# Performance work log

Hardware: AMD Instinct MI355X
Metric: run time of the kernel (lower is better)

Reference implementation:

```python
import jax, jax.numpy as jnp
import numpy as np

ACT_BITS = 8
W_BITS = 8
BN_EPS = 1e-5


def _round_ste(x):
    # straight-through round (HAWQ-style ste_round)
    return x + jax.lax.stop_gradient(jnp.round(x) - x)


def _quant_sym(x, bits):
    # symmetric per-tensor fake quantization; scale treated as constant (EMA min/max in original)
    n = float(2 ** (bits - 1) - 1)
    s = jax.lax.stop_gradient(jnp.maximum(jnp.max(jnp.abs(x)) / n, 1e-8))
    xq = jnp.clip(_round_ste(x / s), -n - 1.0, n) * s
    return xq, s


def _conv(x, w, stride, pad):
    return jax.lax.conv_general_dilated(
        x, w, (stride, stride), [(pad, pad), (pad, pad)],
        dimension_numbers=("NCHW", "OIHW", "NCHW"))


def _quant_bn(x, gamma, beta, mean, var):
    # fold BN into a per-channel scale+bias; quantize the folded scale like a weight
    ws = gamma * jax.lax.rsqrt(var + BN_EPS)          # [C]
    wq, ws_scale = _quant_sym(ws, W_BITS)
    b = beta - mean * wq                               # [C]
    return x * wq[None, :, None, None] + b[None, :, None, None], ws_scale


def setup_inputs() -> dict:
    key = jax.random.key(0)
    ks = jax.random.split(key, 16)
    d = {}
    d["x"] = jax.random.normal(ks[0], (32, 128, 56, 56), jnp.float32)
    d["w1"] = jax.random.normal(ks[1], (256, 128, 3, 3), jnp.float32) * 0.05
    d["w2"] = jax.random.normal(ks[2], (256, 256, 3, 3), jnp.float32) * 0.05
    d["w_id"] = jax.random.normal(ks[3], (256, 128, 1, 1), jnp.float32) * 0.05
    for i, pfx in enumerate(["bn1", "bn2", "id"]):
        k4 = jax.random.split(ks[4 + i], 4)
        d[pfx + "_gamma"] = jax.random.uniform(k4[0], (256,), jnp.float32) + 0.5
        d[pfx + "_beta"] = jax.random.normal(k4[1], (256,), jnp.float32) * 0.1
        d[pfx + "_mean"] = jax.random.normal(k4[2], (256,), jnp.float32) * 0.1
        d[pfx + "_var"] = jax.random.uniform(k4[3], (256,), jnp.float32) + 0.5
    return d


def reference(x, w1, w2, w_id,
              bn1_gamma, bn1_beta, bn1_mean, bn1_var,
              bn2_gamma, bn2_beta, bn2_mean, bn2_var,
              id_gamma, id_beta, id_mean, id_var):
    # quant_act on block input
    xq, act_s = _quant_sym(x, ACT_BITS)

    # identity branch: 1x1 stride-2 quantized conv -> quant_act -> folded quant bn
    w_id_q, _ = _quant_sym(w_id, W_BITS)
    identity = _conv(xq, w_id_q, 2, 0)
    identity, _ = _quant_sym(identity, ACT_BITS)
    identity, _ = _quant_bn(identity, id_gamma, id_beta, id_mean, id_var)

    # main branch conv1 (3x3 stride 2) -> act quant -> bn -> relu -> act quant
    w1_q, _ = _quant_sym(w1, W_BITS)
    h = _conv(xq, w1_q, 2, 1)
    h, _ = _quant_sym(h, ACT_BITS)
    h, _ = _quant_bn(h, bn1_gamma, bn1_beta, bn1_mean, bn1_var)
    h = jax.nn.relu(h)
    h, _ = _quant_sym(h, ACT_BITS)

    # conv2 (3x3 stride 1) -> act quant -> bn
    w2_q, _ = _quant_sym(w2, W_BITS)
    h = _conv(h, w2_q, 1, 1)
    h, _ = _quant_sym(h, ACT_BITS)
    h, _ = _quant_bn(h, bn2_gamma, bn2_beta, bn2_mean, bn2_var)

    # residual add -> int32 requant -> relu
    h = h + identity
    h, out_s = _quant_sym(h, ACT_BITS)
    h = jax.nn.relu(h)
    return h, out_s
```

## Files before the change

### kernel.cpp

```cpp
#include <hip/hip_runtime.h>
#include <limits.h>

#define THREADS 256

typedef int vi4 __attribute__((ext_vector_type(4)));

__device__ __forceinline__ float clamp8f(float q) { return fminf(fmaxf(q, -128.0f), 127.0f); }
__device__ __forceinline__ float sc_from_bits(unsigned b) {
  return fmaxf(__uint_as_float(b) / 127.0f, 1e-8f);
}
__device__ __forceinline__ signed char q8(float v, float s) {
  return (signed char)(int)clamp8f(rintf(v / s));
}


__device__ __forceinline__ void amax_body(const float4* __restrict__ p, int n4, int bid,
                                          int nblocks, unsigned* __restrict__ slot) {
  const int tid = threadIdx.x;
  const int stride = nblocks * THREADS;
  float m = 0.0f;
  int i = bid * THREADS + tid;
  for (; i + 3 * stride < n4; i += 4 * stride) {
    float4 v0 = p[i];
    float4 v1 = p[i + stride];
    float4 v2 = p[i + 2 * stride];
    float4 v3 = p[i + 3 * stride];
    float m0 = fmaxf(fmaxf(fabsf(v0.x), fabsf(v0.y)), fmaxf(fabsf(v0.z), fabsf(v0.w)));
    float m1 = fmaxf(fmaxf(fabsf(v1.x), fabsf(v1.y)), fmaxf(fabsf(v1.z), fabsf(v1.w)));
    float m2 = fmaxf(fmaxf(fabsf(v2.x), fabsf(v2.y)), fmaxf(fabsf(v2.z), fabsf(v2.w)));
    float m3 = fmaxf(fmaxf(fabsf(v3.x), fabsf(v3.y)), fmaxf(fabsf(v3.z), fabsf(v3.w)));
    m = fmaxf(m, fmaxf(fmaxf(m0, m1), fmaxf(m2, m3)));
  }
  for (; i < n4; i += stride) {
    float4 v = p[i];
    m = fmaxf(m, fmaxf(fmaxf(fabsf(v.x), fabsf(v.y)), fmaxf(fabsf(v.z), fabsf(v.w))));
  }
#pragma unroll
  for (int k = 32; k >= 1; k >>= 1) m = fmaxf(m, __shfl_xor(m, k));
  __shared__ float wred[4];
  if ((tid & 63) == 0) wred[tid >> 6] = m;
  __syncthreads();
  if (tid == 0) {
    m = fmaxf(fmaxf(wred[0], wred[1]), fmaxf(wred[2], wred[3]));
    atomicMax(slot, __float_as_uint(m));
  }
}

__global__ __launch_bounds__(THREADS) void k_pre(
    int* IS, const float* g1, const float* be1, const float* m1, const float* v1, float* wq1,
    float* b1, const float* g2, const float* be2, const float* m2, const float* v2, float* wq2,
    float* b2, const float* gi, const float* bei, const float* mi, const float* vvi, float* wqi,
    float* bi, const float4* w1, const float4* w2, const float4* wid, const float4* x) {
  unsigned* ISu = (unsigned*)IS;
  int b = blockIdx.x;
  int c = threadIdx.x;
  if (b < 3) {
    const float *gamma, *beta, *mean, *var;
    float *wq, *bb;
    if (b == 0) { gamma = g1; beta = be1; mean = m1; var = v1; wq = wq1; bb = b1; }
    else if (b == 1) { gamma = g2; beta = be2; mean = m2; var = v2; wq = wq2; bb = b2; }
    else { gamma = gi; beta = bei; mean = mi; var = vvi; wq = wqi; bb = bi; }
    __shared__ float red[THREADS];
    float ws = gamma[c] * (1.0f / sqrtf(var[c] + 1e-5f));
    red[c] = fabsf(ws);
    __syncthreads();
    for (int s = THREADS / 2; s > 0; s >>= 1) {
      if (c < s) red[c] = fmaxf(red[c], red[c + s]);
      __syncthreads();
    }
    float sws = fmaxf(red[0] / 127.0f, 1e-8f);
    float q = clamp8f(rintf(ws / sws)) * sws;
    wq[c] = q;
    bb[c] = beta[c] - mean[c] * q;
    return;
  }
  b -= 3;
  if (b < 64) { amax_body(w1, 73728, b, 64, ISu + 1); return; }
  b -= 64;
  if (b < 128) { amax_body(w2, 147456, b, 128, ISu + 2); return; }
  b -= 128;
  if (b < 16) { amax_body(wid, 8192, b, 16, ISu + 3); return; }
  b -= 16;
  amax_body(x, 3211264, b, 512, ISu + 0);
}

__global__ __launch_bounds__(THREADS) void k_quant(const float* __restrict__ x,
                                                   int* __restrict__ X8,
                                                   const float* __restrict__ w1f,
                                                   vi4* __restrict__ W1m,
                                                   const float* __restrict__ w2f,
                                                   vi4* __restrict__ W2m,
                                                   const float* __restrict__ widf,
                                                   vi4* __restrict__ Widm,
                                                   const unsigned* __restrict__ ISu) {
  __shared__ signed char tile[56 * 132];
  int b = blockIdx.x;
  int t = threadIdx.x;
  if (b < 1792) {
    float s = sc_from_bits(ISu[0]);
    int h = b % 56, n = b / 56;
    const float* xp = x + ((n * 128) * 56 + h) * 56;
#pragma unroll
    for (int k = 0; k < 28; ++k) {
      int i = t + k * 256;
      int w = i % 56, c = i / 56;
      tile[w * 132 + c] = q8(xp[c * 3136 + w], s);
    }
    __syncthreads();
    int* op = X8 + (n * 56 + h) * 56 * 32;
#pragma unroll
    for (int k = 0; k < 7; ++k) {
      int i = t + k * 256;
      int w = i >> 5, c4 = (i & 31) * 4;
      const signed char* tp = tile + w * 132 + c4;
      op[i] = (int)(unsigned char)tp[0] | ((int)(unsigned char)tp[1] << 8) |
              ((int)(unsigned char)tp[2] << 16) | ((int)(unsigned char)tp[3] << 24);
    }
    return;
  }
  if (b < 1864) {
    int tt = (b - 1792) * THREADS + t;
    float s = sc_from_bits(ISu[1]);
    int lane = tt & 63;
    int cotile = (tt >> 6) & 15;
    int ks = tt >> 10;
    int tap = ks >> 1, kc = ks & 1;
    int kh = tap / 3, kw = tap % 3;
    int co = cotile * 16 + (lane & 15);
    int ci0 = kc * 64 + (lane >> 4) * 16;
    const float* src = w1f + (co * 128 + ci0) * 9 + kh * 3 + kw;
    int r[4];
#pragma unroll
    for (int q = 0; q < 4; ++q) {
      unsigned b0 = (unsigned char)q8(src[(q * 4 + 0) * 9], s);
      unsigned b1 = (unsigned char)q8(src[(q * 4 + 1) * 9], s);
      unsigned b2 = (unsigned char)q8(src[(q * 4 + 2) * 9], s);
      unsigned b3 = (unsigned char)q8(src[(q * 4 + 3) * 9], s);
      r[q] = (int)(b0 | (b1 << 8) | (b2 << 16) | (b3 << 24));
    }
    vi4 v = {r[0], r[1], r[2], r[3]};
    W1m[tt] = v;
    return;
  }
  if (b < 2008) {
    int tt = (b - 1864) * THREADS + t;
    float s = sc_from_bits(ISu[2]);
    int lane = tt & 63;
    int cotile = (tt >> 6) & 15;
    int ks = tt >> 10;
    int tap = ks >> 2, kc = ks & 3;
    int kh = tap / 3, kw = tap % 3;
    int co = cotile * 16 + (lane & 15);
    int ci0 = kc * 64 + (lane >> 4) * 16;
    const float* src = w2f + (co * 256 + ci0) * 9 + kh * 3 + kw;
    int r[4];
#pragma unroll
    for (int q = 0; q < 4; ++q) {
      unsigned b0 = (unsigned char)q8(src[(q * 4 + 0) * 9], s);
      unsigned b1 = (unsigned char)q8(src[(q * 4 + 1) * 9], s);
      unsigned b2 = (unsigned char)q8(src[(q * 4 + 2) * 9], s);
      unsigned b3 = (unsigned char)q8(src[(q * 4 + 3) * 9], s);
      r[q] = (int)(b0 | (b1 << 8) | (b2 << 16) | (b3 << 24));
    }
    vi4 v = {r[0], r[1], r[2], r[3]};
    W2m[tt] = v;
    return;
  }
  {
    int tt = (b - 2008) * THREADS + t;
    float s = sc_from_bits(ISu[3]);
    int lane = tt & 63;
    int cotile = (tt >> 6) & 15;
    int ks = tt >> 10;
    int co = cotile * 16 + (lane & 15);
    int ci0 = ks * 64 + (lane >> 4) * 16;
    const float* src = widf + co * 128 + ci0;
    int r[4];
#pragma unroll
    for (int q = 0; q < 4; ++q) {
      unsigned b0 = (unsigned char)q8(src[q * 4 + 0], s);
      unsigned b1 = (unsigned char)q8(src[q * 4 + 1], s);
      unsigned b2 = (unsigned char)q8(src[q * 4 + 2], s);
      unsigned b3 = (unsigned char)q8(src[q * 4 + 3], s);
      r[q] = (int)(b0 | (b1 << 8) | (b2 << 16) | (b3 << 24));
    }
    vi4 v = {r[0], r[1], r[2], r[3]};
    Widm[tt] = v;
  }
}

#define MFMA_I8(a, b, c) __builtin_amdgcn_mfma_i32_16x16x64_i8(a, b, c, 0, 0, 0)

__global__ __launch_bounds__(THREADS, 2) void k_conv1(const int* __restrict__ X8,
                                                      const vi4* __restrict__ W1m,
                                                      const vi4* __restrict__ Widm,
                                                      int* __restrict__ H1, int* __restrict__ IDI,
                                                      int* __restrict__ maxS,
                                                      int* __restrict__ minS,
                                                      int* __restrict__ maxabs_id) {
  __shared__ __align__(16) int lds[5 * 58 * 36];
  __shared__ int sMax[2][128], sMin[2][128], redA[4];
  const int tid = threadIdx.x;
  const int bx = blockIdx.x;
  const int n = bx / 28, rr = bx % 28;
  const int hp = rr >> 1, nh = rr & 1;
  const int ho0 = hp * 2;
  vi4 zero = {0, 0, 0, 0};

  for (int r = 0; r < 5; ++r) {
    int h = 2 * ho0 - 1 + r;
    int* dst = lds + r * 58 * 36;
    if (h >= 0 && h < 56) {
      const vi4* src = (const vi4*)(X8 + (n * 56 + h) * 56 * 32);
      for (int i4 = tid; i4 < 448; i4 += THREADS) {
        int col = i4 >> 3, c = (i4 & 7) * 4;
        *(vi4*)(dst + (col + 1) * 36 + c) = src[i4];
      }
      if (tid < 32) dst[tid] = 0;
      else if (tid >= 128 && tid < 160) dst[57 * 36 + (tid - 128)] = 0;
    } else {
      for (int i4 = tid; i4 < 522; i4 += THREADS) ((vi4*)dst)[i4] = zero;
    }
  }
  __syncthreads();

  const int lane = tid & 63, wv = tid >> 6;
  const int mw = wv & 1, nw = wv >> 1;
  const int lm = lane & 15, quad = lane >> 4;
  const int woc0 = lm, woc1 = (16 + lm) > 27 ? 27 : (16 + lm);
  const int choff = quad * 4;
  const int ho = ho0 + mw;
  const int obase = ((n * 28 + ho) * 28) * 256;
  const int ctbase = nh * 8 + nw * 4;

  vi4 acc[2][4];
  vi4 bcur[4], bnext[4];
  vi4 a0c, a1c, a0n, a1n;

#pragma unroll
  for (int mt = 0; mt < 2; ++mt)
#pragma unroll
    for (int ct = 0; ct < 4; ++ct) acc[mt][ct] = zero;
  const vi4* wibase = Widm + ctbase * 64 + lane;
  {
    const int ro = (2 * mw + 1) * 58;
#pragma unroll
    for (int kc = 0; kc < 2; ++kc) {
      vi4 a0 = *(const vi4*)(lds + (ro + 2 * woc0 + 1) * 36 + kc * 16 + choff);
      vi4 a1 = *(const vi4*)(lds + (ro + 2 * woc1 + 1) * 36 + kc * 16 + choff);
#pragma unroll
      for (int ct = 0; ct < 4; ++ct) {
        vi4 b = wibase[kc * 1024 + ct * 64];
        acc[0][ct] = MFMA_I8(a0, b, acc[0][ct]);
        acc[1][ct] = MFMA_I8(a1, b, acc[1][ct]);
      }
    }
  }
  int am = 0;
#pragma unroll
  for (int ct = 0; ct < 4; ++ct) {
    const int co = (ctbase + ct) * 16 + lm;
#pragma unroll
    for (int mt = 0; mt < 2; ++mt)
#pragma unroll
      for (int r = 0; r < 4; ++r) {
        int wo = mt * 16 + quad * 4 + r;
        if (wo < 28) {
          int v = acc[mt][ct][r];
          IDI[obase + wo * 256 + co] = v;
          am = max(am, v < 0 ? -v : v);
        }
      }
  }
#pragma unroll
  for (int k = 32; k >= 1; k >>= 1) am = max(am, __shfl_xor(am, k));
  if (lane == 0) redA[wv] = am;

#pragma unroll
  for (int mt = 0; mt < 2; ++mt)
#pragma unroll
    for (int ct = 0; ct < 4; ++ct) acc[mt][ct] = zero;
  const vi4* wbase = W1m + ctbase * 64 + lane;
#pragma unroll
  for (int ct = 0; ct < 4; ++ct) bcur[ct] = wbase[ct * 64];
  {
    const int ro = (2 * mw) * 58;
    a0c = *(const vi4*)(lds + (ro + 2 * woc0) * 36 + choff);
    a1c = *(const vi4*)(lds + (ro + 2 * woc1) * 36 + choff);
  }
#pragma unroll 1
  for (int ks = 0; ks < 18; ++ks) {
    int ksn = ks + 1;
    if (ksn < 18) {
      int khn = (ksn >= 6) + (ksn >= 12);
      int t2 = ksn - khn * 6;
      int kwn = t2 >> 1, kcn = t2 & 1;
#pragma unroll
      for (int ct = 0; ct < 4; ++ct) bnext[ct] = wbase[ksn * 1024 + ct * 64];
      int ro = (2 * mw + khn) * 58;
      a0n = *(const vi4*)(lds + (ro + 2 * woc0 + kwn) * 36 + kcn * 16 + choff);
      a1n = *(const vi4*)(lds + (ro + 2 * woc1 + kwn) * 36 + kcn * 16 + choff);
    }
#pragma unroll
    for (int ct = 0; ct < 4; ++ct) {
      acc[0][ct] = MFMA_I8(a0c, bcur[ct], acc[0][ct]);
      acc[1][ct] = MFMA_I8(a1c, bcur[ct], acc[1][ct]);
    }
    a0c = a0n;
    a1c = a1n;
#pragma unroll
    for (int ct = 0; ct < 4; ++ct) bcur[ct] = bnext[ct];
  }

#pragma unroll
  for (int ct = 0; ct < 4; ++ct) {
    const int co = (ctbase + ct) * 16 + lm;
    int vmax = INT_MIN, vmin = INT_MAX;
#pragma unroll
    for (int mt = 0; mt < 2; ++mt)
#pragma unroll
      for (int r = 0; r < 4; ++r) {
        int wo = mt * 16 + quad * 4 + r;
        if (wo < 28) {
          int v = acc[mt][ct][r];
          H1[obase + wo * 256 + co] = v;
          vmax = max(vmax, v);
          vmin = min(vmin, v);
        }
      }
    vmax = max(vmax, __shfl_xor(vmax, 16));
    vmax = max(vmax, __shfl_xor(vmax, 32));
    vmin = min(vmin, __shfl_xor(vmin, 16));
    vmin = min(vmin, __shfl_xor(vmin, 32));
    if (lane < 16) {
      sMax[mw][nw * 64 + ct * 16 + lane] = vmax;
      sMin[mw][nw * 64 + ct * 16 + lane] = vmin;
    }
  }
  __syncthreads();
  if (tid < 128) {
    int row = n * 14 + hp;
    maxS[row * 256 + nh * 128 + tid] = max(sMax[0][tid], sMax[1][tid]);
    minS[row * 256 + nh * 128 + tid] = min(sMin[0][tid], sMin[1][tid]);
  }
  if (tid == 0) {
    int a = max(max(redA[0], redA[1]), max(redA[2], redA[3]));
    atomicMax(maxabs_id, a);
  }
}

__global__ __launch_bounds__(THREADS) void k_rs1(int* __restrict__ IS, float* __restrict__ SC,
                                                 const int* __restrict__ maxS,
                                                 const int* __restrict__ minS,
                                                 const float* __restrict__ wq1,
                                                 const float* __restrict__ b1) {
  __shared__ int ri[THREADS];
  __shared__ float rf[THREADS];
  int c = threadIdx.x;
  int vmax = INT_MIN, vmin = INT_MAX;
#pragma unroll 4
  for (int r = 0; r < 448; ++r) {
    vmax = max(vmax, maxS[r * 256 + c]);
    vmin = min(vmin, minS[r * 256 + c]);
  }
  int a1 = vmax < 0 ? -vmax : vmax;
  int a0 = vmin < 0 ? -vmin : vmin;
  ri[c] = max(a1, a0);
  __syncthreads();
  for (int s = THREADS / 2; s > 0; s >>= 1) {
    if (c < s) ri[c] = max(ri[c], ri[c + s]);
    __syncthreads();
  }
  int mh1 = ri[0];
  const unsigned* ISu = (const unsigned*)IS;
  float sx = sc_from_bits(ISu[0]);
  float sw1 = sc_from_bits(ISu[1]);
  float sxw = sx * sw1;
  float s_h1 = fmaxf(sxw * (float)mh1 / 127.0f, 1e-8f);
  float wq = wq1[c], bbc = b1[c];
  float q1 = clamp8f(rintf((float)vmax * sxw / s_h1));
  float q0 = clamp8f(rintf((float)vmin * sxw / s_h1));
  float hv1 = q1 * s_h1, hv0 = q0 * s_h1;
  float y1 = fmaxf(hv1 * wq + bbc, 0.0f);
  float y0 = fmaxf(hv0 * wq + bbc, 0.0f);
  rf[c] = fmaxf(y1, y0);
  __syncthreads();
  for (int s = THREADS / 2; s > 0; s >>= 1) {
    if (c < s) rf[c] = fmaxf(rf[c], rf[c + s]);
    __syncthreads();
  }
  if (c == 0) {
    IS[4] = mh1;
    SC[7] = rf[0];
    SC[8] = s_h1;
    SC[9] = fmaxf(rf[0] / 127.0f, 1e-8f);
    float swid = sc_from_bits(ISu[3]);
    SC[10] = fmaxf(sx * swid * (float)IS[5] / 127.0f, 1e-8f);
  }
}

__device__ __forceinline__ signed char qact(int v, float sxw, float s_h1, float s_y2, float wq,
                                            float bb) {
  float hf = (float)v * sxw;
  float q = clamp8f(rintf(hf / s_h1));
  float hv = q * s_h1;
  float y = fmaxf(hv * wq + bb, 0.0f);
  float a = fminf(fmaxf(rintf(y / s_y2), -128.0f), 127.0f);
  return (signed char)(int)a;
}

__global__ __launch_bounds__(THREADS) void k_qh1(const int4* __restrict__ H1,
                                                 char4* __restrict__ A2,
                                                 const float* __restrict__ SC,
                                                 const float* __restrict__ wq1,
                                                 const float* __restrict__ b1) {
  int t = blockIdx.x * THREADS + threadIdx.x;
  const unsigned* ISu = (const unsigned*)SC;
  float sx = sc_from_bits(ISu[0]);
  float sw1 = sc_from_bits(ISu[1]);
  float sxw = sx * sw1;
  float s_h1 = SC[8];
  float s_y2 = SC[9];
  int4 v = H1[t];
  int c0 = (t * 4) & 255;
  char4 r;
  r.x = qact(v.x, sxw, s_h1, s_y2, wq1[c0], b1[c0]);
  r.y = qact(v.y, sxw, s_h1, s_y2, wq1[c0 + 1], b1[c0 + 1]);
  r.z = qact(v.z, sxw, s_h1, s_y2, wq1[c0 + 2], b1[c0 + 2]);
  r.w = qact(v.w, sxw, s_h1, s_y2, wq1[c0 + 3], b1[c0 + 3]);
  A2[t] = r;
}

__global__ __launch_bounds__(THREADS, 2) void k_conv2(const int* __restrict__ A2,
                                                      const vi4* __restrict__ W2m,
                                                      int* __restrict__ H2,
                                                      int* __restrict__ maxabs_h2) {
  __shared__ __align__(16) int lds[4 * 30 * 68];
  __shared__ int redA[4];
  const int tid = threadIdx.x;
  const int bx = blockIdx.x;
  const int n = bx / 28, rr = bx % 28;
  const int hp = rr >> 1, nh = rr & 1;
  const int ho0 = hp * 2;
  vi4 zero = {0, 0, 0, 0};

  for (int r = 0; r < 4; ++r) {
    int h = ho0 - 1 + r;
    int* dst = lds + r * 30 * 68;
    if (h >= 0 && h < 28) {
      const vi4* src = (const vi4*)(A2 + (n * 28 + h) * 28 * 64);
      for (int i4 = tid; i4 < 448; i4 += THREADS) {
        int col = i4 >> 4, c = (i4 & 15) * 4;
        *(vi4*)(dst + (col + 1) * 68 + c) = src[i4];
      }
      if (tid < 64) dst[tid] = 0;
      else if (tid >= 128 && tid < 192) dst[29 * 68 + (tid - 128)] = 0;
    } else {
      for (int i4 = tid; i4 < 510; i4 += THREADS) ((vi4*)dst)[i4] = zero;
    }
  }
  __syncthreads();

  const int lane = tid & 63, wv = tid >> 6;
  const int mw = wv & 1, nw = wv >> 1;
  const int lm = lane & 15, quad = lane >> 4;
  const int woc0 = lm, woc1 = (16 + lm) > 27 ? 27 : (16 + lm);
  const int choff = quad * 4;
  const int ho = ho0 + mw;
  const int ctbase = nh * 8 + nw * 4;

  vi4 acc[2][4];
  vi4 bcur[4], bnext[4];
  vi4 a0c, a1c, a0n, a1n;
#pragma unroll
  for (int mt = 0; mt < 2; ++mt)
#pragma unroll
    for (int ct = 0; ct < 4; ++ct) acc[mt][ct] = zero;

  const vi4* wbase = W2m + ctbase * 64 + lane;
#pragma unroll
  for (int ct = 0; ct < 4; ++ct) bcur[ct] = wbase[ct * 64];
  {
    const int ro = mw * 30;
    a0c = *(const vi4*)(lds + (ro + woc0) * 68 + choff);
    a1c = *(const vi4*)(lds + (ro + woc1) * 68 + choff);
  }
#pragma unroll 1
  for (int ks = 0; ks < 36; ++ks) {
    int ksn = ks + 1;
    if (ksn < 36) {
      int khn = (ksn >= 12) + (ksn >= 24);
      int t2 = ksn - khn * 12;
      int kwn = t2 >> 2, kcn = t2 & 3;
#pragma unroll
      for (int ct = 0; ct < 4; ++ct) bnext[ct] = wbase[ksn * 1024 + ct * 64];
      int ro = (mw + khn) * 30;
      a0n = *(const vi4*)(lds + (ro + woc0 + kwn) * 68 + kcn * 16 + choff);
      a1n = *(const vi4*)(lds + (ro + woc1 + kwn) * 68 + kcn * 16 + choff);
    }
#pragma unroll
    for (int ct = 0; ct < 4; ++ct) {
      acc[0][ct] = MFMA_I8(a0c, bcur[ct], acc[0][ct]);
      acc[1][ct] = MFMA_I8(a1c, bcur[ct], acc[1][ct]);
    }
    a0c = a0n;
    a1c = a1n;
#pragma unroll
    for (int ct = 0; ct < 4; ++ct) bcur[ct] = bnext[ct];
  }

  const int obase = ((n * 28 + ho) * 28) * 256;
  int am = 0;
#pragma unroll
  for (int ct = 0; ct < 4; ++ct) {
    const int co = (ctbase + ct) * 16 + lm;
#pragma unroll
    for (int mt = 0; mt < 2; ++mt)
#pragma unroll
      for (int r = 0; r < 4; ++r) {
        int wo = mt * 16 + quad * 4 + r;
        if (wo < 28) {
          int v = acc[mt][ct][r];
          H2[obase + wo * 256 + co] = v;
          am = max(am, v < 0 ? -v : v);
        }
      }
  }
#pragma unroll
  for (int k = 32; k >= 1; k >>= 1) am = max(am, __shfl_xor(am, k));
  if (lane == 0) redA[wv] = am;
  __syncthreads();
  if (tid == 0) {
    int a = max(max(redA[0], redA[1]), max(redA[2], redA[3]));
    atomicMax(maxabs_h2, a);
  }
}

struct SumParams {
  float sxw2, s_h2, sxwid, s_idq;
};
__device__ __forceinline__ float sum_val(int v2, int vi, const SumParams& P, float wq2c, float b2c,
                                         float wqidc, float bidc) {
  float q2 = clamp8f(rintf((float)v2 * P.sxw2 / P.s_h2));
  float z = (q2 * P.s_h2) * wq2c + b2c;
  float qi = clamp8f(rintf((float)vi * P.sxwid / P.s_idq));
  float zi = (qi * P.s_idq) * wqidc + bidc;
  return z + zi;
}
__device__ __forceinline__ SumParams make_params(const float* SC, const int* IS) {
  const unsigned* ISu = (const unsigned*)IS;
  SumParams P;
  float sx = sc_from_bits(ISu[0]);
  float sw2 = sc_from_bits(ISu[2]);
  float swid = sc_from_bits(ISu[3]);
  float s_y2 = SC[9];
  P.s_idq = SC[10];
  P.sxw2 = s_y2 * sw2;
  P.s_h2 = fmaxf(P.sxw2 * (float)IS[6] / 127.0f, 1e-8f);
  P.sxwid = sx * swid;
  return P;
}

__global__ __launch_bounds__(THREADS) void k_absmax2(const int4* __restrict__ H2,
                                                     const int4* __restrict__ IDI,
                                                     const float* __restrict__ SC,
                                                     const int* __restrict__ IS,
                                                     const float* __restrict__ wq2,
                                                     const float* __restrict__ b2,
                                                     const float* __restrict__ wqid,
                                                     const float* __restrict__ bidp,
                                                     unsigned* __restrict__ slot) {
  __shared__ float pw2[256], pb2[256], pwi[256], pbi[256];
  int tid = threadIdx.x;
  pw2[tid] = wq2[tid];
  pb2[tid] = b2[tid];
  pwi[tid] = wqid[tid];
  pbi[tid] = bidp[tid];
  __syncthreads();
  SumParams P = make_params(SC, IS);
  const int n4 = 1605632;
  const int stride = gridDim.x * THREADS;
  float m = 0.0f;
  for (int i = blockIdx.x * THREADS + tid; i < n4; i += stride) {
    int4 v2 = H2[i];
    int4 vi = IDI[i];
    int c0 = (i * 4) & 255;
    m = fmaxf(m, fabsf(sum_val(v2.x, vi.x, P, pw2[c0], pb2[c0], pwi[c0], pbi[c0])));
    m = fmaxf(m, fabsf(sum_val(v2.y, vi.y, P, pw2[c0 + 1], pb2[c0 + 1], pwi[c0 + 1], pbi[c0 + 1])));
    m = fmaxf(m, fabsf(sum_val(v2.z, vi.z, P, pw2[c0 + 2], pb2[c0 + 2], pwi[c0 + 2], pbi[c0 + 2])));
    m = fmaxf(m, fabsf(sum_val(v2.w, vi.w, P, pw2[c0 + 3], pb2[c0 + 3], pwi[c0 + 3], pbi[c0 + 3])));
  }
#pragma unroll
  for (int k = 32; k >= 1; k >>= 1) m = fmaxf(m, __shfl_xor(m, k));
  __shared__ float wred[4];
  if ((tid & 63) == 0) wred[tid >> 6] = m;
  __syncthreads();
  if (tid == 0) {
    m = fmaxf(fmaxf(wred[0], wred[1]), fmaxf(wred[2], wred[3]));
    atomicMax(slot, __float_as_uint(m));
  }
}

__global__ __launch_bounds__(THREADS) void k_out(const int* __restrict__ H2,
                                                 const int* __restrict__ IDI,
                                                 const float* __restrict__ SC,
                                                 const int* __restrict__ IS,
                                                 const float* __restrict__ wq2,
                                                 const float* __restrict__ b2,
                                                 const float* __restrict__ wqid,
                                                 const float* __restrict__ bidp,
                                                 float* __restrict__ out) {
  __shared__ float tile[64 * 57];
  __shared__ float pw2[64], pb2[64], pwi[64], pbi[64];
  int tid = threadIdx.x;
  int b = blockIdx.x;
  int ct = b & 3;
  int rt = (b >> 2) % 14;
  int n = b / 56;
  int c0 = ct * 64;
  int r0 = rt * 56;
  if (tid < 64) {
    pw2[tid] = wq2[c0 + tid];
    pb2[tid] = b2[c0 + tid];
    pwi[tid] = wqid[c0 + tid];
    pbi[tid] = bidp[c0 + tid];
  }
  __syncthreads();
  SumParams P = make_params(SC, IS);
  float out_s = fmaxf(__uint_as_float(((const unsigned*)IS)[11]) / 127.0f, 1e-8f);

  const int base = (n * 784 + r0) * 256 + c0;
#pragma unroll
  for (int k = 0; k < 14; ++k) {
    int idx = tid + k * 256;
    int rl = idx >> 6;
    int cl = idx & 63;
    int e = base + rl * 256 + cl;
    float sv = sum_val(H2[e], IDI[e], P, pw2[cl], pb2[cl], pwi[cl], pbi[cl]);
    float q = clamp8f(rintf(sv / out_s));
    tile[cl * 57 + rl] = q > 0.0f ? q * out_s : 0.0f;
  }
  __syncthreads();
  float* ob = out + n * 200704 + c0 * 784 + r0;
#pragma unroll
  for (int k = 0; k < 14; ++k) {
    int idx = tid + k * 256;
    int cl = idx / 56;
    int rl = idx % 56;
    ob[cl * 784 + rl] = tile[cl * 57 + rl];
  }
  if (b == 0 && tid == 0) out[6422528] = out_s;
}

extern "C" void kernel_launch(void* const* d_in, const int* in_sizes, int n_in, void* d_out,
                              int out_size, void* d_ws, size_t ws_size, hipStream_t stream) {
  (void)in_sizes; (void)n_in; (void)out_size; (void)ws_size;
  const float* x = (const float*)d_in[0];
  const float* w1 = (const float*)d_in[1];
  const float* w2 = (const float*)d_in[2];
  const float* wid = (const float*)d_in[3];
  const float* bn1g = (const float*)d_in[4];
  const float* bn1b = (const float*)d_in[5];
  const float* bn1m = (const float*)d_in[6];
  const float* bn1v = (const float*)d_in[7];
  const float* bn2g = (const float*)d_in[8];
  const float* bn2b = (const float*)d_in[9];
  const float* bn2m = (const float*)d_in[10];
  const float* bn2v = (const float*)d_in[11];
  const float* idg = (const float*)d_in[12];
  const float* idb = (const float*)d_in[13];
  const float* idm = (const float*)d_in[14];
  const float* idv = (const float*)d_in[15];

  char* ws = (char*)d_ws;
  float* SC = (float*)ws;
  int* IS = (int*)ws;
  unsigned* ISu = (unsigned*)ws;
  float* wq1 = (float*)(ws + 3072);
  float* b1 = (float*)(ws + 4096);
  float* wq2 = (float*)(ws + 5120);
  float* b2 = (float*)(ws + 6144);
  float* wqid = (float*)(ws + 7168);
  float* bid = (float*)(ws + 8192);
  char* X8 = ws + 16384;
  char* A2 = X8;
  char* W1m = X8 + 12845056;
  char* W2m = W1m + 294912;
  char* Widm = W2m + 589824;
  int* H1 = (int*)(Widm + 32768);
  int* H2 = H1;
  int* IDI = (int*)((char*)H1 + 25690112);
  float* out = (float*)d_out;
  int* maxS = (int*)d_out;
  int* minS = maxS + 448 * 256;

  hipMemsetAsync(IS, 0, 256, stream);
  k_pre<<<723, THREADS, 0, stream>>>(IS, bn1g, bn1b, bn1m, bn1v, wq1, b1, bn2g, bn2b, bn2m, bn2v,
                                     wq2, b2, idg, idb, idm, idv, wqid, bid, (const float4*)w1,
                                     (const float4*)w2, (const float4*)wid, (const float4*)x);
  k_quant<<<2016, THREADS, 0, stream>>>(x, (int*)X8, w1, (vi4*)W1m, w2, (vi4*)W2m, wid,
                                        (vi4*)Widm, ISu);
  k_conv1<<<896, THREADS, 0, stream>>>((const int*)X8, (const vi4*)W1m, (const vi4*)Widm, H1, IDI,
                                       maxS, minS, IS + 5);
  k_rs1<<<1, THREADS, 0, stream>>>(IS, SC, maxS, minS, wq1, b1);
  k_qh1<<<6272, THREADS, 0, stream>>>((const int4*)H1, (char4*)A2, SC, wq1, b1);
  k_conv2<<<896, THREADS, 0, stream>>>((const int*)A2, (const vi4*)W2m, H2, IS + 6);
  k_absmax2<<<1024, THREADS, 0, stream>>>((const int4*)H2, (const int4*)IDI, SC, IS, wq2, b2, wqid,
                                          bid, ISu + 11);
  k_out<<<1792, THREADS, 0, stream>>>(H2, IDI, SC, IS, wq2, b2, wqid, bid, out);
}
```

Measured before the change: 271.2 us.

## Ping-pong register double buffering in convs, widen rs1 reduction, raise occupancy bounds

Both conv kernels' K loops now unroll by two and use explicit A/B register buffers, so the next operands load while the current MFMAs issue and the per-iteration register copies disappear. Launch-bound minimum occupancy rises to 3 for conv1 and 4 for conv2, which may force register limits and spills. The single-block k_rs1 reduction now uses 1024 threads that each scan a quarter of the rows, then combines the partials in shared memory, shortening its serial column scan.

```diff
diff --git a/kernel.cpp b/kernel.cpp
--- a/kernel.cpp
+++ b/kernel.cpp
@@ -191,7 +191,7 @@
 
 #define MFMA_I8(a, b, c) __builtin_amdgcn_mfma_i32_16x16x64_i8(a, b, c, 0, 0, 0)
 
-__global__ __launch_bounds__(THREADS, 2) void k_conv1(const int* __restrict__ X8,
+__global__ __launch_bounds__(THREADS, 3) void k_conv1(const int* __restrict__ X8,
                                                       const vi4* __restrict__ W1m,
                                                       const vi4* __restrict__ Widm,
                                                       int* __restrict__ H1, int* __restrict__ IDI,
@@ -234,8 +234,8 @@
   const int ctbase = nh * 8 + nw * 4;
 
   vi4 acc[2][4];
-  vi4 bcur[4], bnext[4];
-  vi4 a0c, a1c, a0n, a1n;
+  vi4 bA[4], bB[4];
+  vi4 a0A, a1A, a0B, a1B;
 
 #pragma unroll
   for (int mt = 0; mt < 2; ++mt)
@@ -282,34 +282,46 @@
     for (int ct = 0; ct < 4; ++ct) acc[mt][ct] = zero;
   const vi4* wbase = W1m + ctbase * 64 + lane;
 #pragma unroll
-  for (int ct = 0; ct < 4; ++ct) bcur[ct] = wbase[ct * 64];
+  for (int ct = 0; ct < 4; ++ct) bA[ct] = wbase[ct * 64];
   {
     const int ro = (2 * mw) * 58;
-    a0c = *(const vi4*)(lds + (ro + 2 * woc0) * 36 + choff);
-    a1c = *(const vi4*)(lds + (ro + 2 * woc1) * 36 + choff);
+    a0A = *(const vi4*)(lds + (ro + 2 * woc0) * 36 + choff);
+    a1A = *(const vi4*)(lds + (ro + 2 * woc1) * 36 + choff);
   }
 #pragma unroll 1
-  for (int ks = 0; ks < 18; ++ks) {
-    int ksn = ks + 1;
-    if (ksn < 18) {
-      int khn = (ksn >= 6) + (ksn >= 12);
-      int t2 = ksn - khn * 6;
-      int kwn = t2 >> 1, kcn = t2 & 1;
-#pragma unroll
-      for (int ct = 0; ct < 4; ++ct) bnext[ct] = wbase[ksn * 1024 + ct * 64];
-      int ro = (2 * mw + khn) * 58;
-      a0n = *(const vi4*)(lds + (ro + 2 * woc0 + kwn) * 36 + kcn * 16 + choff);
-      a1n = *(const vi4*)(lds + (ro + 2 * woc1 + kwn) * 36 + kcn * 16 + choff);
+  for (int ks = 0; ks < 18; ks += 2) {
+    {
+      const int ksn = ks + 1;
+      const int khn = (ksn >= 6) + (ksn >= 12);
+      const int t2 = ksn - khn * 6;
+      const int kwn = t2 >> 1, kcn = t2 & 1;
+#pragma unroll
+      for (int ct = 0; ct < 4; ++ct) bB[ct] = wbase[ksn * 1024 + ct * 64];
+      const int ro = (2 * mw + khn) * 58;
+      a0B = *(const vi4*)(lds + (ro + 2 * woc0 + kwn) * 36 + kcn * 16 + choff);
+      a1B = *(const vi4*)(lds + (ro + 2 * woc1 + kwn) * 36 + kcn * 16 + choff);
     }
 #pragma unroll
     for (int ct = 0; ct < 4; ++ct) {
-      acc[0][ct] = MFMA_I8(a0c, bcur[ct], acc[0][ct]);
-      acc[1][ct] = MFMA_I8(a1c, bcur[ct], acc[1][ct]);
-    }
-    a0c = a0n;
-    a1c = a1n;
-#pragma unroll
-    for (int ct = 0; ct < 4; ++ct) bcur[ct] = bnext[ct];
+      acc[0][ct] = MFMA_I8(a0A, bA[ct], acc[0][ct]);
+      acc[1][ct] = MFMA_I8(a1A, bA[ct], acc[1][ct]);
+    }
+    if (ks + 2 < 18) {
+      const int ksn = ks + 2;
+      const int khn = (ksn >= 6) + (ksn >= 12);
+      const int t2 = ksn - khn * 6;
+      const int kwn = t2 >> 1, kcn = t2 & 1;
+#pragma unroll
+      for (int ct = 0; ct < 4; ++ct) bA[ct] = wbase[ksn * 1024 + ct * 64];
+      const int ro = (2 * mw + khn) * 58;
+      a0A = *(const vi4*)(lds + (ro + 2 * woc0 + kwn) * 36 + kcn * 16 + choff);
+      a1A = *(const vi4*)(lds + (ro + 2 * woc1 + kwn) * 36 + kcn * 16 + choff);
+    }
+#pragma unroll
+    for (int ct = 0; ct < 4; ++ct) {
+      acc[0][ct] = MFMA_I8(a0B, bB[ct], acc[0][ct]);
+      acc[1][ct] = MFMA_I8(a1B, bB[ct], acc[1][ct]);
+    }
   }
 
 #pragma unroll
@@ -349,26 +361,35 @@
   }
 }
 
-__global__ __launch_bounds__(THREADS) void k_rs1(int* __restrict__ IS, float* __restrict__ SC,
-                                                 const int* __restrict__ maxS,
-                                                 const int* __restrict__ minS,
-                                                 const float* __restrict__ wq1,
-                                                 const float* __restrict__ b1) {
-  __shared__ int ri[THREADS];
-  __shared__ float rf[THREADS];
-  int c = threadIdx.x;
+__global__ __launch_bounds__(1024) void k_rs1(int* __restrict__ IS, float* __restrict__ SC,
+                                              const int* __restrict__ maxS,
+                                              const int* __restrict__ minS,
+                                              const float* __restrict__ wq1,
+                                              const float* __restrict__ b1) {
+  __shared__ int pMax[4][256], pMin[4][256];
+  __shared__ int ri[256];
+  __shared__ float rf[256];
+  int t = threadIdx.x;
+  int c = t & 255, part = t >> 8;
   int vmax = INT_MIN, vmin = INT_MAX;
 #pragma unroll 4
-  for (int r = 0; r < 448; ++r) {
+  for (int r = part; r < 448; r += 4) {
     vmax = max(vmax, maxS[r * 256 + c]);
     vmin = min(vmin, minS[r * 256 + c]);
   }
-  int a1 = vmax < 0 ? -vmax : vmax;
-  int a0 = vmin < 0 ? -vmin : vmin;
-  ri[c] = max(a1, a0);
-  __syncthreads();
-  for (int s = THREADS / 2; s > 0; s >>= 1) {
-    if (c < s) ri[c] = max(ri[c], ri[c + s]);
+  pMax[part][c] = vmax;
+  pMin[part][c] = vmin;
+  __syncthreads();
+  if (t < 256) {
+    vmax = max(max(pMax[0][c], pMax[1][c]), max(pMax[2][c], pMax[3][c]));
+    vmin = min(min(pMin[0][c], pMin[1][c]), min(pMin[2][c], pMin[3][c]));
+    int a1 = vmax < 0 ? -vmax : vmax;
+    int a0 = vmin < 0 ? -vmin : vmin;
+    ri[c] = max(a1, a0);
+  }
+  __syncthreads();
+  for (int s = 128; s > 0; s >>= 1) {
+    if (t < s) ri[t] = max(ri[t], ri[t + s]);
     __syncthreads();
   }
   int mh1 = ri[0];
@@ -377,19 +398,21 @@
   float sw1 = sc_from_bits(ISu[1]);
   float sxw = sx * sw1;
   float s_h1 = fmaxf(sxw * (float)mh1 / 127.0f, 1e-8f);
-  float wq = wq1[c], bbc = b1[c];
-  float q1 = clamp8f(rintf((float)vmax * sxw / s_h1));
-  float q0 = clamp8f(rintf((float)vmin * sxw / s_h1));
-  float hv1 = q1 * s_h1, hv0 = q0 * s_h1;
-  float y1 = fmaxf(hv1 * wq + bbc, 0.0f);
-  float y0 = fmaxf(hv0 * wq + bbc, 0.0f);
-  rf[c] = fmaxf(y1, y0);
-  __syncthreads();
-  for (int s = THREADS / 2; s > 0; s >>= 1) {
-    if (c < s) rf[c] = fmaxf(rf[c], rf[c + s]);
+  if (t < 256) {
+    float wq = wq1[c], bbc = b1[c];
+    float q1 = clamp8f(rintf((float)vmax * sxw / s_h1));
+    float q0 = clamp8f(rintf((float)vmin * sxw / s_h1));
+    float hv1 = q1 * s_h1, hv0 = q0 * s_h1;
+    float y1 = fmaxf(hv1 * wq + bbc, 0.0f);
+    float y0 = fmaxf(hv0 * wq + bbc, 0.0f);
+    rf[c] = fmaxf(y1, y0);
+  }
+  __syncthreads();
+  for (int s = 128; s > 0; s >>= 1) {
+    if (t < s) rf[t] = fmaxf(rf[t], rf[t + s]);
     __syncthreads();
   }
-  if (c == 0) {
+  if (t == 0) {
     IS[4] = mh1;
     SC[7] = rf[0];
     SC[8] = s_h1;
@@ -431,7 +454,7 @@
   A2[t] = r;
 }
 
-__global__ __launch_bounds__(THREADS, 2) void k_conv2(const int* __restrict__ A2,
+__global__ __launch_bounds__(THREADS, 4) void k_conv2(const int* __restrict__ A2,
                                                       const vi4* __restrict__ W2m,
                                                       int* __restrict__ H2,
                                                       int* __restrict__ maxabs_h2) {
@@ -470,8 +493,8 @@
   const int ctbase = nh * 8 + nw * 4;
 
   vi4 acc[2][4];
-  vi4 bcur[4], bnext[4];
-  vi4 a0c, a1c, a0n, a1n;
+  vi4 bA[4], bB[4];
+  vi4 a0A, a1A, a0B, a1B;
 #pragma unroll
   for (int mt = 0; mt < 2; ++mt)
 #pragma unroll
@@ -479,34 +502,46 @@
 
   const vi4* wbase = W2m + ctbase * 64 + lane;
 #pragma unroll
-  for (int ct = 0; ct < 4; ++ct) bcur[ct] = wbase[ct * 64];
+  for (int ct = 0; ct < 4; ++ct) bA[ct] = wbase[ct * 64];
   {
     const int ro = mw * 30;
-    a0c = *(const vi4*)(lds + (ro + woc0) * 68 + choff);
-    a1c = *(const vi4*)(lds + (ro + woc1) * 68 + choff);
+    a0A = *(const vi4*)(lds + (ro + woc0) * 68 + choff);
+    a1A = *(const vi4*)(lds + (ro + woc1) * 68 + choff);
   }
 #pragma unroll 1
-  for (int ks = 0; ks < 36; ++ks) {
-    int ksn = ks + 1;
-    if (ksn < 36) {
-      int khn = (ksn >= 12) + (ksn >= 24);
-      int t2 = ksn - khn * 12;
-      int kwn = t2 >> 2, kcn = t2 & 3;
-#pragma unroll
-      for (int ct = 0; ct < 4; ++ct) bnext[ct] = wbase[ksn * 1024 + ct * 64];
-      int ro = (mw + khn) * 30;
-      a0n = *(const vi4*)(lds + (ro + woc0 + kwn) * 68 + kcn * 16 + choff);
-      a1n = *(const vi4*)(lds + (ro + woc1 + kwn) * 68 + kcn * 16 + choff);
+  for (int ks = 0; ks < 36; ks += 2) {
+    {
+      const int ksn = ks + 1;
+      const int khn = (ksn >= 12) + (ksn >= 24);
+      const int t2 = ksn - khn * 12;
+      const int kwn = t2 >> 2, kcn = t2 & 3;
+#pragma unroll
+      for (int ct = 0; ct < 4; ++ct) bB[ct] = wbase[ksn * 1024 + ct * 64];
+      const int ro = (mw + khn) * 30;
+      a0B = *(const vi4*)(lds + (ro + woc0 + kwn) * 68 + kcn * 16 + choff);
+      a1B = *(const vi4*)(lds + (ro + woc1 + kwn) * 68 + kcn * 16 + choff);
     }
 #pragma unroll
     for (int ct = 0; ct < 4; ++ct) {
-      acc[0][ct] = MFMA_I8(a0c, bcur[ct], acc[0][ct]);
-      acc[1][ct] = MFMA_I8(a1c, bcur[ct], acc[1][ct]);
-    }
-    a0c = a0n;
-    a1c = a1n;
-#pragma unroll
-    for (int ct = 0; ct < 4; ++ct) bcur[ct] = bnext[ct];
+      acc[0][ct] = MFMA_I8(a0A, bA[ct], acc[0][ct]);
+      acc[1][ct] = MFMA_I8(a1A, bA[ct], acc[1][ct]);
+    }
+    if (ks + 2 < 36) {
+      const int ksn = ks + 2;
+      const int khn = (ksn >= 12) + (ksn >= 24);
+      const int t2 = ksn - khn * 12;
+      const int kwn = t2 >> 2, kcn = t2 & 3;
+#pragma unroll
+      for (int ct = 0; ct < 4; ++ct) bA[ct] = wbase[ksn * 1024 + ct * 64];
+      const int ro = (mw + khn) * 30;
+      a0A = *(const vi4*)(lds + (ro + woc0 + kwn) * 68 + kcn * 16 + choff);
+      a1A = *(const vi4*)(lds + (ro + woc1 + kwn) * 68 + kcn * 16 + choff);
+    }
+#pragma unroll
+    for (int ct = 0; ct < 4; ++ct) {
+      acc[0][ct] = MFMA_I8(a0B, bB[ct], acc[0][ct]);
+      acc[1][ct] = MFMA_I8(a1B, bB[ct], acc[1][ct]);
+    }
   }
 
   const int obase = ((n * 28 + ho) * 28) * 256;
@@ -702,7 +737,7 @@
                                         (vi4*)Widm, ISu);
   k_conv1<<<896, THREADS, 0, stream>>>((const int*)X8, (const vi4*)W1m, (const vi4*)Widm, H1, IDI,
                                        maxS, minS, IS + 5);
-  k_rs1<<<1, THREADS, 0, stream>>>(IS, SC, maxS, minS, wq1, b1);
+  k_rs1<<<1, 1024, 0, stream>>>(IS, SC, maxS, minS, wq1, b1);
   k_qh1<<<6272, THREADS, 0, stream>>>((const int4*)H1, (char4*)A2, SC, wq1, b1);
   k_conv2<<<896, THREADS, 0, stream>>>((const int*)A2, (const vi4*)W2m, H2, IS + 6);
   k_absmax2<<<1024, THREADS, 0, stream>>>((const int4*)H2, (const int4*)IDI, SC, IS, wq2, b2, wqid,
```

Result: faster. 256.9 us (-5.3%).
